# Kernel optimization log

Hardware: AMD Instinct MI355X
Metric: run time of the kernel (lower is better)

## Reference

```python
import jax, jax.numpy as jnp
import numpy as np

NUM_TOKENS = 2048  # = token_limit(0.5) * seq_len(4096)


def setup_inputs() -> dict:
    key = jax.random.key(0)
    k0, k1, k2, k3 = jax.random.split(key, 4)
    B, S, D, F = 4, 4096, 2048, 8192
    return {
        "x": jax.random.normal(k0, (B, S, D), dtype=jnp.float32),
        "Wp": jax.random.normal(k1, (D, 1), dtype=jnp.float32) * (1.0 / np.sqrt(D)),
        "bp": jnp.zeros((1,), dtype=jnp.float32),
        "W1": jax.random.normal(k2, (D, F), dtype=jnp.float32) * (1.0 / np.sqrt(D)),
        "b1": jnp.zeros((F,), dtype=jnp.float32),
        "W2": jax.random.normal(k3, (F, D), dtype=jnp.float32) * (1.0 / np.sqrt(F)),
        "b2": jnp.zeros((D,), dtype=jnp.float32),
    }


def reference(x, Wp, bp, W1, b1, W2, b2):
    # Router: per-token scalar score via Linear(dim, 1)
    weights = x @ Wp + bp                      # [B, S, 1]
    # Faithful to source: softmax over dim=-1 (size-1 axis -> all ones)
    weights = jax.nn.softmax(weights, axis=-1)  # [B, S, 1]
    scores = weights[..., 0]                   # [B, S]
    # top-k token selection along the sequence axis
    _, idx = jax.lax.top_k(scores, NUM_TOKENS)  # [B, k] int32
    # gather the selected full tokens (intended semantics of the expand+gather)
    topk_tokens = jnp.take_along_axis(x, idx[:, :, None], axis=1)  # [B, k, D]
    # downstream block: transformer FFN
    h = jax.nn.gelu(topk_tokens @ W1 + b1)     # [B, k, 4D]
    out = h @ W2 + b2                          # [B, k, D]
    return out
```

## Files before the change

kernel.cpp:

```cpp
#include <hip/hip_runtime.h>
#include <hip/hip_bf16.h>

typedef unsigned int u32;
typedef unsigned short u16;

using bf16x8 = __attribute__((ext_vector_type(8))) short;
using f32x4  = __attribute__((ext_vector_type(4))) float;

#define DEVI static __device__ __forceinline__

DEVI u16 f2bf(float f) {
  __hip_bfloat16 h = __float2bfloat16(f);
  union { __hip_bfloat16 h; u16 u; } v; v.h = h;
  return v.u;
}

__global__ void k_convert_x(const float* __restrict__ x, u16* __restrict__ xb) {
  int idx = blockIdx.x * blockDim.x + threadIdx.x;
  size_t e = (size_t)idx * 4;
  int row = (int)(e >> 11);
  int d   = (int)(e & 2047);
  int b = row >> 11, t = row & 2047;
  const float4 v = *reinterpret_cast<const float4*>(
      x + ((size_t)(b * 4096 + t) * 2048 + d));
  ushort4 o;
  o.x = f2bf(v.x); o.y = f2bf(v.y); o.z = f2bf(v.z); o.w = f2bf(v.w);
  *reinterpret_cast<ushort4*>(xb + (size_t)row * 2048 + d) = o;
}

__global__ void k_transpose_bf16(const float* __restrict__ in,
                                 u16* __restrict__ out, int R, int C) {
  __shared__ u16 lds[64][66];
  const int t = threadIdx.x;
  const int tile_r = blockIdx.y * 64;
  const int tile_c = blockIdx.x * 64;
  const int cc = (t & 15) * 4;
  const int r0 = t >> 4;
#pragma unroll
  for (int i = 0; i < 4; ++i) {
    int r = r0 + i * 16;
    const float4 v = *reinterpret_cast<const float4*>(
        in + (size_t)(tile_r + r) * C + tile_c + cc);
    lds[r][cc]     = f2bf(v.x);
    lds[r][cc + 1] = f2bf(v.y);
    lds[r][cc + 2] = f2bf(v.z);
    lds[r][cc + 3] = f2bf(v.w);
  }
  __syncthreads();
  const int rr = (t & 15) * 4;
  const int c0 = t >> 4;
#pragma unroll
  for (int i = 0; i < 4; ++i) {
    int c = c0 + i * 16;
    ushort4 o;
    o.x = lds[rr][c]; o.y = lds[rr + 1][c];
    o.z = lds[rr + 2][c]; o.w = lds[rr + 3][c];
    *reinterpret_cast<ushort4*>(out + (size_t)(tile_c + c) * R + tile_r + rr) = o;
  }
}

#define GLDS16(g, l)                                                          \
  __builtin_amdgcn_global_load_lds(                                           \
      (const __attribute__((address_space(1))) u32*)(g),                      \
      (__attribute__((address_space(3))) u32*)(l), 16, 0, 0)

template <int DO_GELU>
DEVI void gemm_body(u16* lds, const u16* __restrict__ A,
                    const u16* __restrict__ B, const float* __restrict__ bias,
                    void* __restrict__ Cout, int M, int N, int K, int sft) {
  const int bid   = blockIdx.x;
  const int local = bid >> 3;
  const int bn    = ((bid & 7) << sft) + (local & ((1 << sft) - 1));
  const int bm    = local >> sft;

  const int tid  = threadIdx.x;
  const int w    = tid >> 6, lane = tid & 63;
  const int wr   = w >> 2, wcol = w & 3;
  const int l15  = lane & 15, lhi = lane >> 4;

  const size_t arow0 = (size_t)bm * 256;
  const size_t brow0 = (size_t)bn * 256;

  const int srow  = tid >> 3;
  const int scolb = ((tid & 7) * 16) ^ ((srow & 7) << 4);
  const u16* pA = A + (arow0 + srow) * (size_t)K + (scolb >> 1);
  const u16* pB = B + (brow0 + srow) * (size_t)K + (scolb >> 1);
  const int wA = w * 512;

  const u32 arow_b = (u32)((wr * 128 + l15) * 128);
  const u32 brow_b = (u32)((wcol * 64 + l15) * 128);
  const u32 axor   = (u32)((lhi * 16) ^ ((l15 & 7) << 4));
  const char* ldsb = (const char*)lds;

  f32x4 acc[8][4] = {};
  const int nk = K >> 6;

#define STAGE_PAIR(KT, PB, C)                                                 \
  do {                                                                        \
    GLDS16(pA + (size_t)(KT) * 64 + (size_t)(C) * 64 * (size_t)K,             \
           lds + (PB) * 16384 + (C) * 4096 + wA);                             \
    GLDS16(pB + (size_t)(KT) * 64 + (size_t)(C) * 64 * (size_t)K,             \
           lds + 32768 + (PB) * 16384 + (C) * 4096 + wA);                     \
  } while (0)

#define READ_A(MH, ABASE)                                                     \
  _Pragma("unroll") for (int m2 = 0; m2 < 4; ++m2)                            \
  _Pragma("unroll") for (int kk = 0; kk < 2; ++kk)                            \
    afr[m2][kk] = *(const bf16x8*)(ldsb + (ABASE) + arow_b +                  \
                                   ((MH)*4 + m2) * 2048 + (axor ^ (kk << 6)));

#define READ_B(DST, NH, BBASE)                                                \
  _Pragma("unroll") for (int n2 = 0; n2 < 2; ++n2)                            \
  _Pragma("unroll") for (int kk = 0; kk < 2; ++kk)                            \
    DST[n2][kk] = *(const bf16x8*)(ldsb + (BBASE) + brow_b +                  \
                                   ((NH)*2 + n2) * 2048 + (axor ^ (kk << 6)));

#define MFMA_Q(MH, NH, BREG)                                                  \
  _Pragma("unroll") for (int m2 = 0; m2 < 4; ++m2)                            \
  _Pragma("unroll") for (int n2 = 0; n2 < 2; ++n2)                            \
  _Pragma("unroll") for (int kk = 0; kk < 2; ++kk)                            \
    acc[(MH)*4 + m2][(NH)*2 + n2] = __builtin_amdgcn_mfma_f32_16x16x32_bf16(  \
        afr[m2][kk], BREG[n2][kk], acc[(MH)*4 + m2][(NH)*2 + n2], 0, 0, 0);

  STAGE_PAIR(0, 0, 0); STAGE_PAIR(0, 0, 1);
  STAGE_PAIR(0, 0, 2); STAGE_PAIR(0, 0, 3);
  if (nk > 1) {
    STAGE_PAIR(1, 1, 0); STAGE_PAIR(1, 1, 1);
    asm volatile("s_waitcnt vmcnt(4)" ::: "memory");
  } else {
    asm volatile("s_waitcnt vmcnt(0)" ::: "memory");
  }
  __builtin_amdgcn_s_barrier();

  for (int kt = 0; kt < nk; ++kt) {
    const int p = kt & 1;
    const u32 abase = (u32)p * 32768u;
    const u32 bbase = 65536u + (u32)p * 32768u;
    bf16x8 afr[4][2], b0[2][2], b1[2][2];

    READ_A(0, abase);
    READ_B(b0, 0, bbase);
    if (kt + 1 < nk) STAGE_PAIR(kt + 1, p ^ 1, 2);
    __builtin_amdgcn_s_barrier();
    __builtin_amdgcn_s_setprio(1);
    MFMA_Q(0, 0, b0);
    __builtin_amdgcn_s_setprio(0);
    __builtin_amdgcn_s_barrier();

    READ_B(b1, 1, bbase);
    if (kt + 1 < nk) STAGE_PAIR(kt + 1, p ^ 1, 3);
    __builtin_amdgcn_s_barrier();
    __builtin_amdgcn_s_setprio(1);
    MFMA_Q(0, 1, b1);
    __builtin_amdgcn_s_setprio(0);
    __builtin_amdgcn_s_barrier();

    READ_A(1, abase);
    __builtin_amdgcn_s_barrier();
    __builtin_amdgcn_s_setprio(1);
    MFMA_Q(1, 1, b1);
    __builtin_amdgcn_s_setprio(0);
    __builtin_amdgcn_s_barrier();

    __builtin_amdgcn_s_setprio(1);
    MFMA_Q(1, 0, b0);
    __builtin_amdgcn_s_setprio(0);
    __builtin_amdgcn_s_barrier();

    if (kt + 2 < nk) {
      STAGE_PAIR(kt + 2, p, 0); STAGE_PAIR(kt + 2, p, 1);
      asm volatile("s_waitcnt vmcnt(4)" ::: "memory");
    } else {
      asm volatile("s_waitcnt vmcnt(0)" ::: "memory");
    }
    __builtin_amdgcn_s_barrier();
  }

  const int colb = (int)brow0 + wcol * 64;
  float bb[4];
#pragma unroll
  for (int n = 0; n < 4; ++n) bb[n] = bias[colb + n * 16 + l15];
  const int tr = lane >> 2, tc = (lane & 3) * 16;

  if (DO_GELU) {
    u16* slot = lds + (size_t)w * 1152;
#pragma unroll
    for (int m = 0; m < 8; ++m) {
      const int rowb = (int)arow0 + wr * 128 + m * 16;
#pragma unroll
      for (int n = 0; n < 4; ++n)
#pragma unroll
        for (int r = 0; r < 4; ++r) {
          float v = acc[m][n][r] + bb[n];
          float u2 = v * (1.5957691216f + 0.0713548162f * v * v);
          float g  = v / (1.f + __expf(-u2));
          slot[(lhi * 4 + r) * 72 + n * 16 + l15] = f2bf(g);
        }
      asm volatile("s_waitcnt lgkmcnt(0)" ::: "memory");
      uint4 d0 = *(const uint4*)(slot + tr * 72 + tc);
      uint4 d1 = *(const uint4*)(slot + tr * 72 + tc + 8);
      u16* gp = (u16*)Cout + (size_t)(rowb + tr) * N + colb + tc;
      *(uint4*)gp = d0;
      *(uint4*)(gp + 8) = d1;
      asm volatile("s_waitcnt lgkmcnt(0)" ::: "memory");
    }
  } else {
    float* slotf = (float*)(void*)lds + (size_t)w * 1088;
#pragma unroll
    for (int m = 0; m < 8; ++m) {
      const int rowb = (int)arow0 + wr * 128 + m * 16;
#pragma unroll
      for (int n = 0; n < 4; ++n)
#pragma unroll
        for (int r = 0; r < 4; ++r)
          slotf[(lhi * 4 + r) * 68 + n * 16 + l15] = acc[m][n][r] + bb[n];
      asm volatile("s_waitcnt lgkmcnt(0)" ::: "memory");
      float4 f0 = *(const float4*)(slotf + tr * 68 + tc);
      float4 f1 = *(const float4*)(slotf + tr * 68 + tc + 4);
      float4 f2 = *(const float4*)(slotf + tr * 68 + tc + 8);
      float4 f3 = *(const float4*)(slotf + tr * 68 + tc + 12);
      float* gp = (float*)Cout + (size_t)(rowb + tr) * N + colb + tc;
      *(float4*)gp = f0;
      *(float4*)(gp + 4) = f1;
      *(float4*)(gp + 8) = f2;
      *(float4*)(gp + 12) = f3;
      asm volatile("s_waitcnt lgkmcnt(0)" ::: "memory");
    }
  }
#undef STAGE_PAIR
#undef READ_A
#undef READ_B
#undef MFMA_Q
}

__global__ __launch_bounds__(512, 2) void k_ffn1(
    const u16* __restrict__ A, const u16* __restrict__ B,
    const float* __restrict__ bias, void* __restrict__ Cout,
    int M, int N, int K, int sft) {
  __shared__ __align__(64) u16 lds[65536];
  gemm_body<1>(lds, A, B, bias, Cout, M, N, K, sft);
}

__global__ __launch_bounds__(512, 2) void k_ffn2(
    const u16* __restrict__ A, const u16* __restrict__ B,
    const float* __restrict__ bias, void* __restrict__ Cout,
    int M, int N, int K, int sft) {
  __shared__ __align__(64) u16 lds[65536];
  gemm_body<0>(lds, A, B, bias, Cout, M, N, K, sft);
}

extern "C" void kernel_launch(void* const* d_in, const int* in_sizes, int n_in,
                              void* d_out, int out_size, void* d_ws,
                              size_t ws_size, hipStream_t stream) {
  const float* x  = (const float*)d_in[0];
  const float* W1 = (const float*)d_in[3];
  const float* b1 = (const float*)d_in[4];
  const float* W2 = (const float*)d_in[5];
  const float* b2 = (const float*)d_in[6];
  float* out = (float*)d_out;

  char* ws = (char*)d_ws;
  u16* Xb  = (u16*)(ws);
  u16* W1T = (u16*)(ws + 33554432);
  u16* W2T = (u16*)(ws + 67108864);
  u16* H   = (u16*)(ws + 100663296);

  k_convert_x<<<16384, 256, 0, stream>>>(x, Xb);
  k_transpose_bf16<<<dim3(8192 / 64, 2048 / 64), 256, 0, stream>>>(W1, W1T, 2048, 8192);
  k_transpose_bf16<<<dim3(2048 / 64, 8192 / 64), 256, 0, stream>>>(W2, W2T, 8192, 2048);
  k_ffn1<<<1024, 512, 0, stream>>>(Xb, W1T, b1, (void*)H, 8192, 8192, 2048, 2);
  k_ffn2<<<256, 512, 0, stream>>>(H, W2T, b2, (void*)out, 8192, 2048, 8192, 0);
}
```

Before: 575.6 us.

## Restructure GEMM main loop into two-phase schedule and remap FFN2 tile order

The K-loop now issues all LDS fragment reads (A and B halves) up front, then runs the MFMAs in two phases separated by a single barrier, instead of four barrier-separated quarter phases. The next-stage global-to-LDS copies are issued earlier. This cuts the number of workgroup barriers per iteration and gives more room to overlap memory with compute. The cost is extra registers for a second A fragment set, which can lower occupancy. Separately, the FFN2 kernel uses a new block-to-tile mapping that spreads consecutive tiles across the 8 XCD-interleaved block indices, aiming for better L2 locality.

```diff
diff --git a/kernel.cpp b/kernel.cpp
--- a/kernel.cpp
+++ b/kernel.cpp
@@ -64,14 +64,21 @@
       (const __attribute__((address_space(1))) u32*)(g),                      \
       (__attribute__((address_space(3))) u32*)(l), 16, 0, 0)
 
-template <int DO_GELU>
+template <int DO_GELU, int BNPART>
 DEVI void gemm_body(u16* lds, const u16* __restrict__ A,
                     const u16* __restrict__ B, const float* __restrict__ bias,
-                    void* __restrict__ Cout, int M, int N, int K, int sft) {
-  const int bid   = blockIdx.x;
-  const int local = bid >> 3;
-  const int bn    = ((bid & 7) << sft) + (local & ((1 << sft) - 1));
-  const int bm    = local >> sft;
+                    void* __restrict__ Cout, int M, int N, int K, int nbn,
+                    int sft) {
+  const int bid = blockIdx.x;
+  int bm, bn;
+  if (BNPART) {
+    const int local = bid >> 3;
+    bn = ((bid & 7) << sft) + (local & ((1 << sft) - 1));
+    bm = local >> sft;
+  } else {
+    const int wg = (bid & 7) * (gridDim.x >> 3) + (bid >> 3);
+    bm = wg / nbn; bn = wg % nbn;
+  }
 
   const int tid  = threadIdx.x;
   const int w    = tid >> 6, lane = tid & 63;
@@ -103,10 +110,10 @@
            lds + 32768 + (PB) * 16384 + (C) * 4096 + wA);                     \
   } while (0)
 
-#define READ_A(MH, ABASE)                                                     \
+#define READ_A(DST, MH, ABASE)                                                \
   _Pragma("unroll") for (int m2 = 0; m2 < 4; ++m2)                            \
   _Pragma("unroll") for (int kk = 0; kk < 2; ++kk)                            \
-    afr[m2][kk] = *(const bf16x8*)(ldsb + (ABASE) + arow_b +                  \
+    DST[m2][kk] = *(const bf16x8*)(ldsb + (ABASE) + arow_b +                  \
                                    ((MH)*4 + m2) * 2048 + (axor ^ (kk << 6)));
 
 #define READ_B(DST, NH, BBASE)                                                \
@@ -115,12 +122,12 @@
     DST[n2][kk] = *(const bf16x8*)(ldsb + (BBASE) + brow_b +                  \
                                    ((NH)*2 + n2) * 2048 + (axor ^ (kk << 6)));
 
-#define MFMA_Q(MH, NH, BREG)                                                  \
+#define MFMA_Q(MH, NH, AREG, BREG)                                            \
   _Pragma("unroll") for (int m2 = 0; m2 < 4; ++m2)                            \
   _Pragma("unroll") for (int n2 = 0; n2 < 2; ++n2)                            \
   _Pragma("unroll") for (int kk = 0; kk < 2; ++kk)                            \
     acc[(MH)*4 + m2][(NH)*2 + n2] = __builtin_amdgcn_mfma_f32_16x16x32_bf16(  \
-        afr[m2][kk], BREG[n2][kk], acc[(MH)*4 + m2][(NH)*2 + n2], 0, 0, 0);
+        AREG[m2][kk], BREG[n2][kk], acc[(MH)*4 + m2][(NH)*2 + n2], 0, 0, 0);
 
   STAGE_PAIR(0, 0, 0); STAGE_PAIR(0, 0, 1);
   STAGE_PAIR(0, 0, 2); STAGE_PAIR(0, 0, 3);
@@ -136,39 +143,31 @@
     const int p = kt & 1;
     const u32 abase = (u32)p * 32768u;
     const u32 bbase = 65536u + (u32)p * 32768u;
-    bf16x8 afr[4][2], b0[2][2], b1[2][2];
-
-    READ_A(0, abase);
+    bf16x8 a0[4][2], a1[4][2], b0[2][2], b1[2][2];
+
+    READ_A(a0, 0, abase);
     READ_B(b0, 0, bbase);
-    if (kt + 1 < nk) STAGE_PAIR(kt + 1, p ^ 1, 2);
+    READ_B(b1, 1, bbase);
+    READ_A(a1, 1, abase);
+    if (kt + 1 < nk) { STAGE_PAIR(kt + 1, p ^ 1, 2); STAGE_PAIR(kt + 1, p ^ 1, 3); }
+    __builtin_amdgcn_sched_barrier(0);
+
+    __builtin_amdgcn_s_setprio(1);
+    MFMA_Q(0, 0, a0, b0);
+    MFMA_Q(0, 1, a0, b1);
+    __builtin_amdgcn_s_setprio(0);
+
+    asm volatile("s_waitcnt lgkmcnt(0)" ::: "memory");
     __builtin_amdgcn_s_barrier();
+    __builtin_amdgcn_sched_barrier(0);
+    if (kt + 2 < nk) { STAGE_PAIR(kt + 2, p, 0); STAGE_PAIR(kt + 2, p, 1); }
+
     __builtin_amdgcn_s_setprio(1);
-    MFMA_Q(0, 0, b0);
+    MFMA_Q(1, 1, a1, b1);
+    MFMA_Q(1, 0, a1, b0);
     __builtin_amdgcn_s_setprio(0);
-    __builtin_amdgcn_s_barrier();
-
-    READ_B(b1, 1, bbase);
-    if (kt + 1 < nk) STAGE_PAIR(kt + 1, p ^ 1, 3);
-    __builtin_amdgcn_s_barrier();
-    __builtin_amdgcn_s_setprio(1);
-    MFMA_Q(0, 1, b1);
-    __builtin_amdgcn_s_setprio(0);
-    __builtin_amdgcn_s_barrier();
-
-    READ_A(1, abase);
-    __builtin_amdgcn_s_barrier();
-    __builtin_amdgcn_s_setprio(1);
-    MFMA_Q(1, 1, b1);
-    __builtin_amdgcn_s_setprio(0);
-    __builtin_amdgcn_s_barrier();
-
-    __builtin_amdgcn_s_setprio(1);
-    MFMA_Q(1, 0, b0);
-    __builtin_amdgcn_s_setprio(0);
-    __builtin_amdgcn_s_barrier();
 
     if (kt + 2 < nk) {
-      STAGE_PAIR(kt + 2, p, 0); STAGE_PAIR(kt + 2, p, 1);
       asm volatile("s_waitcnt vmcnt(4)" ::: "memory");
     } else {
       asm volatile("s_waitcnt vmcnt(0)" ::: "memory");
@@ -236,17 +235,17 @@
 __global__ __launch_bounds__(512, 2) void k_ffn1(
     const u16* __restrict__ A, const u16* __restrict__ B,
     const float* __restrict__ bias, void* __restrict__ Cout,
-    int M, int N, int K, int sft) {
+    int M, int N, int K, int nbn, int sft) {
   __shared__ __align__(64) u16 lds[65536];
-  gemm_body<1>(lds, A, B, bias, Cout, M, N, K, sft);
+  gemm_body<1, 1>(lds, A, B, bias, Cout, M, N, K, nbn, sft);
 }
 
 __global__ __launch_bounds__(512, 2) void k_ffn2(
     const u16* __restrict__ A, const u16* __restrict__ B,
     const float* __restrict__ bias, void* __restrict__ Cout,
-    int M, int N, int K, int sft) {
+    int M, int N, int K, int nbn, int sft) {
   __shared__ __align__(64) u16 lds[65536];
-  gemm_body<0>(lds, A, B, bias, Cout, M, N, K, sft);
+  gemm_body<0, 0>(lds, A, B, bias, Cout, M, N, K, nbn, sft);
 }
 
 extern "C" void kernel_launch(void* const* d_in, const int* in_sizes, int n_in,
@@ -268,6 +267,6 @@
   k_convert_x<<<16384, 256, 0, stream>>>(x, Xb);
   k_transpose_bf16<<<dim3(8192 / 64, 2048 / 64), 256, 0, stream>>>(W1, W1T, 2048, 8192);
   k_transpose_bf16<<<dim3(2048 / 64, 8192 / 64), 256, 0, stream>>>(W2, W2T, 8192, 2048);
-  k_ffn1<<<1024, 512, 0, stream>>>(Xb, W1T, b1, (void*)H, 8192, 8192, 2048, 2);
-  k_ffn2<<<256, 512, 0, stream>>>(H, W2T, b2, (void*)out, 8192, 2048, 8192, 0);
-}
+  k_ffn1<<<1024, 512, 0, stream>>>(Xb, W1T, b1, (void*)H, 8192, 8192, 2048, 32, 2);
+  k_ffn2<<<256, 512, 0, stream>>>(H, W2T, b2, (void*)out, 8192, 2048, 8192, 8, 0);
+}
```

After: 530.8 us. -7.8%, faster.
